# Kernel tuning notes

Hardware: AMD Instinct MI355X
Metric: run time of the kernel (lower is better)

## Reference

```python
import jax, jax.numpy as jnp
import numpy as np

B = 262144
D = 26  # lip_dim + pose_dim
OUT = 512


def setup_inputs() -> dict:
    key = jax.random.key(0)
    k1, k2 = jax.random.split(key)
    input = jax.random.normal(k1, (B, D), dtype=jnp.float32)
    weight = jax.random.normal(k2, (OUT, D), dtype=jnp.float32)
    return {"input": input, "weight": weight}


def reference(input, weight):
    # weight: [512, d]; reduced QR -> Q: [512, d]
    w = weight + 1e-8
    Q, _ = jnp.linalg.qr(w)
    # torch: sum(diag_embed(input) @ Q.T, dim=1) == input @ Q.T  -> [B, 512]
    out = jnp.einsum('bd,od->bo', input, Q)
    return out
```

## Files before the change

kernel.cpp:

```cpp
#include <hip/hip_runtime.h>
#include <math.h>

#define QR_M 512
#define QR_N 26
#define OUTC 512
#define LDP 30

using half8_t = __attribute__((ext_vector_type(8))) _Float16;
using f32x4   = __attribute__((ext_vector_type(4))) float;

__global__ __launch_bounds__(256, 2) void fused_dir(const float* __restrict__ w,
                                                    const float* __restrict__ x,
                                                    float* __restrict__ out,
                                                    int nblk32) {
  const int tid = threadIdx.x;
  const int l   = tid & 63;
  const int wid = tid >> 6;

  __shared__ float Gs[QR_N][LDP];
  __shared__ float Rt[QR_N][LDP];
  __shared__ float Gp[2][91][4];
  __shared__ __align__(16) _Float16 Qs[QR_M][32];
  __shared__ float tile[4][16 * 132];

  float a0[QR_N], a1[QR_N];
  {
    const float2* w0 = reinterpret_cast<const float2*>(w + (size_t)tid * QR_N);
    const float2* w1 = reinterpret_cast<const float2*>(w + (size_t)(tid + 256) * QR_N);
#pragma unroll
    for (int i = 0; i < 13; ++i) {
      const float2 v0 = w0[i], v1 = w1[i];
      a0[2 * i]     = v0.x + 1e-8f; a0[2 * i + 1] = v0.y + 1e-8f;
      a1[2 * i]     = v1.x + 1e-8f; a1[2 * i + 1] = v1.y + 1e-8f;
    }
  }

  if (tid < 182) {
    const int chunk = tid / 91;
    const int blk   = tid - chunk * 91;
    int cb = 0, rem = blk;
    while (rem >= 13 - cb) { rem -= 13 - cb; ++cb; }
    const int db = cb + rem;
    const int c0 = 2 * cb, d0 = 2 * db;
    float s00 = 0.f, s01 = 0.f, s10 = 0.f, s11 = 0.f;
    const float* wr = w + (size_t)chunk * 256 * QR_N;
    for (int r = 0; r < 256; ++r) {
      float2 ac = *reinterpret_cast<const float2*>(wr + r * QR_N + c0);
      float2 ad = *reinterpret_cast<const float2*>(wr + r * QR_N + d0);
      ac.x += 1e-8f; ac.y += 1e-8f; ad.x += 1e-8f; ad.y += 1e-8f;
      s00 += ac.x * ad.x; s01 += ac.x * ad.y;
      s10 += ac.y * ad.x; s11 += ac.y * ad.y;
    }
    Gp[chunk][blk][0] = s00; Gp[chunk][blk][1] = s01;
    Gp[chunk][blk][2] = s10; Gp[chunk][blk][3] = s11;
  }
  __syncthreads();

  if (tid < 91) {
    int cb = 0, rem = tid;
    while (rem >= 13 - cb) { rem -= 13 - cb; ++cb; }
    const int db = cb + rem;
#pragma unroll
    for (int v = 0; v < 4; ++v) {
      const float s = Gp[0][tid][v] + Gp[1][tid][v];
      const int c = 2 * cb + (v >> 1);
      const int d = 2 * db + (v & 1);
      Gs[c][d] = s;
      Gs[d][c] = s;
    }
  }
  __syncthreads();

  if (wid == 0) {
    const int c  = l;
    const int cm = (c < QR_N) ? c : (QR_N - 1);
    float gcol[QR_N], tcol[QR_N], rcol[QR_N];
#pragma unroll
    for (int r = 0; r < QR_N; ++r) gcol[r] = Gs[r][cm];
#pragma unroll
    for (int r = 0; r < QR_N; ++r) tcol[r] = w[r * QR_N + cm] + 1e-8f;
#pragma unroll
    for (int r = 0; r < QR_N; ++r) rcol[r] = 0.0f;

#pragma unroll
    for (int j = 0; j < QR_N; ++j) {
      float tg = gcol[j];
#pragma unroll
      for (int r = 0; r < QR_N; ++r) {
        if (r < j) tg -= __shfl(rcol[r], j) * rcol[r];
      }
      const float nsq   = __shfl(tg, j);
      const float alpha = __shfl(tcol[j], j);
      const float norm  = sqrtf(nsq);
      const float beta  = (alpha >= 0.0f) ? -norm : norm;
      const float tau   = (beta - alpha) / beta;
      const float scale = 1.0f / (alpha - beta);
      const float wc    = (tg - beta * tcol[j]) * scale;
      const float tw    = (c > j) ? (tau * wc) : 0.0f;
      tcol[j] -= tw;
      rcol[j]  = (c == j) ? beta : tcol[j];
#pragma unroll
      for (int rr = 0; rr < QR_N; ++rr) {
        if (rr > j) {
          const float vtop = __shfl(tcol[rr], j) * scale;
          tcol[rr] -= tw * vtop;
        }
      }
      if (c >= j && c < QR_N) Rt[c][j] = rcol[j];
    }
  }
  __syncthreads();

  {
    float rinv[QR_N];
#pragma unroll
    for (int cc = 0; cc < QR_N; ++cc) rinv[cc] = 1.0f / Rt[cc][cc];

    float y0[QR_N], y1[QR_N];
#pragma unroll
    for (int cc = 0; cc < QR_N; ++cc) { y0[cc] = a0[cc]; y1[cc] = a1[cc]; }
#pragma unroll
    for (int cc = 0; cc < QR_N; ++cc) {
      float s0 = y0[cc], s1 = y1[cc];
      int k = 0;
#pragma unroll
      for (; k + 1 < cc; k += 2) {
        const float2 rk = *reinterpret_cast<const float2*>(&Rt[cc][k]);
        s0 -= y0[k] * rk.x + y0[k + 1] * rk.y;
        s1 -= y1[k] * rk.x + y1[k + 1] * rk.y;
      }
      if (k < cc) { const float rk = Rt[cc][k]; s0 -= y0[k] * rk; s1 -= y1[k] * rk; }
      y0[cc] = s0 * rinv[cc];
      y1[cc] = s1 * rinv[cc];
    }

    half8_t h[4];
#pragma unroll
    for (int e = 0; e < 8; ++e) h[0][e] = (_Float16)y0[e];
#pragma unroll
    for (int e = 0; e < 8; ++e) h[1][e] = (_Float16)y0[8 + e];
#pragma unroll
    for (int e = 0; e < 8; ++e) h[2][e] = (_Float16)y0[16 + e];
    h[3][0] = (_Float16)y0[24]; h[3][1] = (_Float16)y0[25];
#pragma unroll
    for (int e = 2; e < 8; ++e) h[3][e] = (_Float16)0.0f;
    half8_t* q0 = reinterpret_cast<half8_t*>(&Qs[tid][0]);
    q0[0] = h[0]; q0[1] = h[1]; q0[2] = h[2]; q0[3] = h[3];

#pragma unroll
    for (int e = 0; e < 8; ++e) h[0][e] = (_Float16)y1[e];
#pragma unroll
    for (int e = 0; e < 8; ++e) h[1][e] = (_Float16)y1[8 + e];
#pragma unroll
    for (int e = 0; e < 8; ++e) h[2][e] = (_Float16)y1[16 + e];
    h[3][0] = (_Float16)y1[24]; h[3][1] = (_Float16)y1[25];
#pragma unroll
    for (int e = 2; e < 8; ++e) h[3][e] = (_Float16)0.0f;
    half8_t* q1 = reinterpret_cast<half8_t*>(&Qs[tid + 256][0]);
    q1[0] = h[0]; q1[1] = h[1]; q1[2] = h[2]; q1[3] = h[3];
  }
  __syncthreads();

  const int rloc  = l & 15;
  const int grp   = l >> 4;
  const int k0    = grp * 8;
  const int rhalf = (wid >> 1) * 16;
  const int chalf = (wid & 1) * 256;
  const int t2b   = (wid & 1) * 16;
  float* tw = tile[wid];

  half8_t bq[16];
#pragma unroll
  for (int t2 = 0; t2 < 16; ++t2)
    bq[t2] = *reinterpret_cast<const half8_t*>(&Qs[(t2b + t2) * 16 + rloc][k0]);

  for (int rb = blockIdx.x; rb < nblk32; rb += gridDim.x) {
    const int row = rb * 32 + rhalf + rloc;
    half8_t av;
    const float* xp = x + (size_t)row * QR_N + k0;
    if (grp < 3) {
#pragma unroll
      for (int e = 0; e < 4; ++e) {
        float2 v = *reinterpret_cast<const float2*>(xp + 2 * e);
        av[2 * e]     = (_Float16)v.x;
        av[2 * e + 1] = (_Float16)v.y;
      }
    } else {
      float2 v = *reinterpret_cast<const float2*>(xp);
      av[0] = (_Float16)v.x; av[1] = (_Float16)v.y;
#pragma unroll
      for (int e = 2; e < 8; ++e) av[e] = (_Float16)0.0f;
    }

#pragma unroll
    for (int cc = 0; cc < 2; ++cc) {
#pragma unroll
      for (int tt = 0; tt < 8; ++tt) {
        f32x4 acc = {0.0f, 0.0f, 0.0f, 0.0f};
        acc = __builtin_amdgcn_mfma_f32_16x16x32_f16(av, bq[cc * 8 + tt], acc, 0, 0, 0);
#pragma unroll
        for (int j = 0; j < 4; ++j)
          tw[(grp * 4 + j) * 132 + tt * 16 + rloc] = acc[j];
      }
      __syncthreads();
#pragma unroll
      for (int it = 0; it < 8; ++it) {
        const int r  = it * 2 + (l >> 5);
        const int cg = l & 31;
        f32x4 v = *reinterpret_cast<const f32x4*>(&tw[r * 132 + 4 * cg]);
        *reinterpret_cast<f32x4*>(
            out + (size_t)(rb * 32 + rhalf + r) * OUTC + chalf + cc * 128 + 4 * cg) = v;
      }
      __syncthreads();
    }
  }
}

extern "C" void kernel_launch(void* const* d_in, const int* in_sizes, int n_in,
                              void* d_out, int out_size, void* d_ws, size_t ws_size,
                              hipStream_t stream) {
  const float* input  = (const float*)d_in[0];
  const float* weight = (const float*)d_in[1];
  float* out = (float*)d_out;

  const int B = in_sizes[0] / QR_N;
  const int nblk32 = B / 32;

  fused_dir<<<512, 256, 0, stream>>>(weight, input, out, nblk32);
}
```

Before: 146.1 us.

## Split Gram computation into separate kernel, alias shared memory, raise occupancy

Moves the 512x26 Gram-matrix reduction out of the fused kernel into a small pre-kernel that writes 16 partial Gram blocks to workspace; the main kernel sums those partials instead of each block redundantly scanning the whole weight matrix. Shared memory is packed into one buffer, with the output staging tile aliasing the Gs/Rt/Qs region once Q has been loaded into registers. This allows launch bounds of 4 blocks per CU and a grid of 1024 blocks. Output stores become nontemporal. The cost is an extra kernel launch plus a workspace round trip, and the QR and triangular solve are still repeated in every block.

After: 151.2 us. +3.5%, slower.

```diff
diff --git a/kernel.cpp b/kernel.cpp
--- a/kernel.cpp
+++ b/kernel.cpp
@@ -9,65 +9,73 @@
 using half8_t = __attribute__((ext_vector_type(8))) _Float16;
 using f32x4   = __attribute__((ext_vector_type(4))) float;
 
-__global__ __launch_bounds__(256, 2) void fused_dir(const float* __restrict__ w,
+__global__ __launch_bounds__(448) void gram_part(const float* __restrict__ w,
+                                                 float* __restrict__ gp) {
+  __shared__ float Ab[32][27];
+  const int tid = threadIdx.x;
+  const int b   = blockIdx.x;
+  if (tid < 416) {
+    const int r  = tid / 13;
+    const int c2 = tid - r * 13;
+    const float2 v = *reinterpret_cast<const float2*>(
+        w + (size_t)(b * 32 + r) * QR_N + 2 * c2);
+    Ab[r][2 * c2]     = v.x + 1e-8f;
+    Ab[r][2 * c2 + 1] = v.y + 1e-8f;
+  }
+  __syncthreads();
+  if (tid < 351) {
+    int cb = 0, rem = tid;
+    while (rem >= QR_N - cb) { rem -= QR_N - cb; ++cb; }
+    const int d = cb + rem;
+    float s = 0.0f;
+#pragma unroll
+    for (int r = 0; r < 32; ++r) s += Ab[r][cb] * Ab[r][d];
+    gp[b * 351 + tid] = s;
+  }
+}
+
+#define SM_GS   0
+#define SM_RT   3200
+#define SM_QS   6400
+#define SM_SIZE 39168
+
+__global__ __launch_bounds__(256, 4) void fused_dir(const float* __restrict__ w,
+                                                    const float* __restrict__ gp,
                                                     const float* __restrict__ x,
                                                     float* __restrict__ out,
                                                     int nblk32) {
+  __shared__ __align__(16) char smem[SM_SIZE];
+  float*    Gs   = reinterpret_cast<float*>(smem + SM_GS);
+  float*    Rt   = reinterpret_cast<float*>(smem + SM_RT);
+  _Float16* Qs   = reinterpret_cast<_Float16*>(smem + SM_QS);
+  float*    tile = reinterpret_cast<float*>(smem);
+
   const int tid = threadIdx.x;
   const int l   = tid & 63;
   const int wid = tid >> 6;
 
-  __shared__ float Gs[QR_N][LDP];
-  __shared__ float Rt[QR_N][LDP];
-  __shared__ float Gp[2][91][4];
-  __shared__ __align__(16) _Float16 Qs[QR_M][32];
-  __shared__ float tile[4][16 * 132];
-
-  float a0[QR_N], a1[QR_N];
+  float y0[QR_N], y1[QR_N];
   {
     const float2* w0 = reinterpret_cast<const float2*>(w + (size_t)tid * QR_N);
     const float2* w1 = reinterpret_cast<const float2*>(w + (size_t)(tid + 256) * QR_N);
 #pragma unroll
     for (int i = 0; i < 13; ++i) {
       const float2 v0 = w0[i], v1 = w1[i];
-      a0[2 * i]     = v0.x + 1e-8f; a0[2 * i + 1] = v0.y + 1e-8f;
-      a1[2 * i]     = v1.x + 1e-8f; a1[2 * i + 1] = v1.y + 1e-8f;
-    }
-  }
-
-  if (tid < 182) {
-    const int chunk = tid / 91;
-    const int blk   = tid - chunk * 91;
-    int cb = 0, rem = blk;
-    while (rem >= 13 - cb) { rem -= 13 - cb; ++cb; }
-    const int db = cb + rem;
-    const int c0 = 2 * cb, d0 = 2 * db;
-    float s00 = 0.f, s01 = 0.f, s10 = 0.f, s11 = 0.f;
-    const float* wr = w + (size_t)chunk * 256 * QR_N;
-    for (int r = 0; r < 256; ++r) {
-      float2 ac = *reinterpret_cast<const float2*>(wr + r * QR_N + c0);
-      float2 ad = *reinterpret_cast<const float2*>(wr + r * QR_N + d0);
-      ac.x += 1e-8f; ac.y += 1e-8f; ad.x += 1e-8f; ad.y += 1e-8f;
-      s00 += ac.x * ad.x; s01 += ac.x * ad.y;
-      s10 += ac.y * ad.x; s11 += ac.y * ad.y;
-    }
-    Gp[chunk][blk][0] = s00; Gp[chunk][blk][1] = s01;
-    Gp[chunk][blk][2] = s10; Gp[chunk][blk][3] = s11;
-  }
-  __syncthreads();
-
-  if (tid < 91) {
-    int cb = 0, rem = tid;
-    while (rem >= 13 - cb) { rem -= 13 - cb; ++cb; }
-    const int db = cb + rem;
-#pragma unroll
-    for (int v = 0; v < 4; ++v) {
-      const float s = Gp[0][tid][v] + Gp[1][tid][v];
-      const int c = 2 * cb + (v >> 1);
-      const int d = 2 * db + (v & 1);
-      Gs[c][d] = s;
-      Gs[d][c] = s;
-    }
+      y0[2 * i] = v0.x + 1e-8f; y0[2 * i + 1] = v0.y + 1e-8f;
+      y1[2 * i] = v1.x + 1e-8f; y1[2 * i + 1] = v1.y + 1e-8f;
+    }
+  }
+
+#pragma unroll
+  for (int p = tid; p < 351; p += 256) {
+    float acc = 0.0f;
+#pragma unroll
+    for (int b = 0; b < 16; ++b) acc += gp[b * 351 + p];
+    int cb = 0, rem = p;
+    while (rem >= QR_N - cb) { rem -= QR_N - cb; ++cb; }
+    const int d = cb + rem;
+    Gs[cb * LDP + d] = acc;
+    Gs[d * LDP + cb] = acc;
   }
   __syncthreads();
 
@@ -76,7 +84,7 @@
     const int cm = (c < QR_N) ? c : (QR_N - 1);
     float gcol[QR_N], tcol[QR_N], rcol[QR_N];
 #pragma unroll
-    for (int r = 0; r < QR_N; ++r) gcol[r] = Gs[r][cm];
+    for (int r = 0; r < QR_N; ++r) gcol[r] = Gs[r * LDP + cm];
 #pragma unroll
     for (int r = 0; r < QR_N; ++r) tcol[r] = w[r * QR_N + cm] + 1e-8f;
 #pragma unroll
@@ -106,7 +114,7 @@
           tcol[rr] -= tw * vtop;
         }
       }
-      if (c >= j && c < QR_N) Rt[c][j] = rcol[j];
+      if (c >= j && c < QR_N) Rt[c * LDP + j] = rcol[j];
     }
   }
   __syncthreads();
@@ -114,22 +122,19 @@
   {
     float rinv[QR_N];
 #pragma unroll
-    for (int cc = 0; cc < QR_N; ++cc) rinv[cc] = 1.0f / Rt[cc][cc];
-
-    float y0[QR_N], y1[QR_N];
-#pragma unroll
-    for (int cc = 0; cc < QR_N; ++cc) { y0[cc] = a0[cc]; y1[cc] = a1[cc]; }
+    for (int cc = 0; cc < QR_N; ++cc) rinv[cc] = 1.0f / Rt[cc * LDP + cc];
+
 #pragma unroll
     for (int cc = 0; cc < QR_N; ++cc) {
       float s0 = y0[cc], s1 = y1[cc];
       int k = 0;
 #pragma unroll
       for (; k + 1 < cc; k += 2) {
-        const float2 rk = *reinterpret_cast<const float2*>(&Rt[cc][k]);
+        const float2 rk = *reinterpret_cast<const float2*>(&Rt[cc * LDP + k]);
         s0 -= y0[k] * rk.x + y0[k + 1] * rk.y;
         s1 -= y1[k] * rk.x + y1[k + 1] * rk.y;
       }
-      if (k < cc) { const float rk = Rt[cc][k]; s0 -= y0[k] * rk; s1 -= y1[k] * rk; }
+      if (k < cc) { const float rk = Rt[cc * LDP + k]; s0 -= y0[k] * rk; s1 -= y1[k] * rk; }
       y0[cc] = s0 * rinv[cc];
       y1[cc] = s1 * rinv[cc];
     }
@@ -144,7 +149,7 @@
     h[3][0] = (_Float16)y0[24]; h[3][1] = (_Float16)y0[25];
 #pragma unroll
     for (int e = 2; e < 8; ++e) h[3][e] = (_Float16)0.0f;
-    half8_t* q0 = reinterpret_cast<half8_t*>(&Qs[tid][0]);
+    half8_t* q0 = reinterpret_cast<half8_t*>(Qs + (size_t)tid * 32);
     q0[0] = h[0]; q0[1] = h[1]; q0[2] = h[2]; q0[3] = h[3];
 
 #pragma unroll
@@ -156,7 +161,7 @@
     h[3][0] = (_Float16)y1[24]; h[3][1] = (_Float16)y1[25];
 #pragma unroll
     for (int e = 2; e < 8; ++e) h[3][e] = (_Float16)0.0f;
-    half8_t* q1 = reinterpret_cast<half8_t*>(&Qs[tid + 256][0]);
+    half8_t* q1 = reinterpret_cast<half8_t*>(Qs + (size_t)(tid + 256) * 32);
     q1[0] = h[0]; q1[1] = h[1]; q1[2] = h[2]; q1[3] = h[3];
   }
   __syncthreads();
@@ -167,12 +172,14 @@
   const int rhalf = (wid >> 1) * 16;
   const int chalf = (wid & 1) * 256;
   const int t2b   = (wid & 1) * 16;
-  float* tw = tile[wid];
 
   half8_t bq[16];
 #pragma unroll
   for (int t2 = 0; t2 < 16; ++t2)
-    bq[t2] = *reinterpret_cast<const half8_t*>(&Qs[(t2b + t2) * 16 + rloc][k0]);
+    bq[t2] = *reinterpret_cast<const half8_t*>(Qs + (size_t)((t2b + t2) * 16 + rloc) * 32 + k0);
+  __syncthreads();
+
+  float* tw = tile + wid * (16 * 132);
 
   for (int rb = blockIdx.x; rb < nblk32; rb += gridDim.x) {
     const int row = rb * 32 + rhalf + rloc;
@@ -208,8 +215,9 @@
         const int r  = it * 2 + (l >> 5);
         const int cg = l & 31;
         f32x4 v = *reinterpret_cast<const f32x4*>(&tw[r * 132 + 4 * cg]);
-        *reinterpret_cast<f32x4*>(
-            out + (size_t)(rb * 32 + rhalf + r) * OUTC + chalf + cc * 128 + 4 * cg) = v;
+        __builtin_nontemporal_store(
+            v, reinterpret_cast<f32x4*>(
+                   out + (size_t)(rb * 32 + rhalf + r) * OUTC + chalf + cc * 128 + 4 * cg));
       }
       __syncthreads();
     }
@@ -222,9 +230,11 @@
   const float* input  = (const float*)d_in[0];
   const float* weight = (const float*)d_in[1];
   float* out = (float*)d_out;
+  float* gp  = (float*)d_ws;
 
   const int B = in_sizes[0] / QR_N;
   const int nblk32 = B / 32;
 
-  fused_dir<<<512, 256, 0, stream>>>(weight, input, out, nblk32);
+  gram_part<<<16, 448, 0, stream>>>(weight, gp);
+  fused_dir<<<1024, 256, 0, stream>>>(weight, gp, input, out, nblk32);
 }
```
